# Kernel optimization log

Measured on AMD Instinct MI355X. Metric: run time of the kernel, lower is better.

The kernel has to match this reference:

```python
import jax, jax.numpy as jnp
import numpy as np

BETA = 0.25
TASK_LR = 1.0
EMBED_DIM = 256
DICT_SIZES = [64, 128, 256, 512]


def setup_inputs() -> dict:
    key = jax.random.key(0)
    ks = jax.random.split(key, 6)
    inp = {
        "x": jax.random.normal(ks[0], (16, 64, 64, EMBED_DIM), dtype=jnp.float32),
        "alpha_vq": jax.random.normal(ks[1], (4,), dtype=jnp.float32),
    }
    # RandomUniform default range (-0.05, 0.05)
    for i, n in enumerate(DICT_SIZES):
        inp[f"dict_{6 + i}"] = jax.random.uniform(
            ks[2 + i], (EMBED_DIM, n), dtype=jnp.float32, minval=-0.05, maxval=0.05
        )
    return inp


def _quantize(flat, dic):
    # flat: [N, D], dic: [D, K]
    sim = flat @ dic  # [N, K]
    dists = (
        jnp.sum(flat * flat, axis=1, keepdims=True)
        + jnp.sum(dic * dic, axis=0, keepdims=True)
        - 2.0 * sim
    )
    idx = jnp.argmin(dists, axis=1)  # [N]
    # equivalent to one_hot(idx) @ dic.T, but as a direct gather
    return jnp.take(dic.T, idx, axis=0)  # [N, D]


def reference(x, alpha_vq, dict_6, dict_7, dict_8, dict_9):
    dicts = [dict_6, dict_7, dict_8, dict_9]
    sg = jax.lax.stop_gradient
    alpha = jax.nn.softmax(alpha_vq)  # [4]
    flat = x.reshape(-1, EMBED_DIM)  # [N, D]

    qs, dict_losses, commit_losses = [], [], []
    for dic in dicts:
        q = _quantize(flat, dic)
        qs.append(q)
        dict_losses.append(jnp.mean(jnp.square(sg(flat) - q)))
        commit_losses.append(jnp.mean(jnp.square(flat - sg(q))))

    loss = jnp.sum(jnp.stack(dict_losses) * alpha) + BETA * jnp.sum(
        jnp.stack(commit_losses) * alpha
    )

    weighted_q = jnp.sum(jnp.stack(qs, axis=0) * alpha[:, None, None], axis=0)
    weighted_q = (TASK_LR * weighted_q).reshape(x.shape)
    # straight-through estimator
    weighted_q = x + sg(weighted_q - x)
    return weighted_q, loss
```

## Files before the change

### kernel.cpp

```cpp
#include <hip/hip_runtime.h>
#include <float.h>
#include <math.h>

#define D 256
#define NROWS 65536
#define RPB 64
#define EPS_CAND 0.02f
#define CAP 6
#define WSFRAG 1024
#define WSDT   246784
#define ASTRIDE 520


typedef __attribute__((ext_vector_type(8)))  short short8v;
typedef __attribute__((ext_vector_type(16))) float f32x16;
typedef __attribute__((ext_vector_type(4)))  float float4v;
typedef __attribute__((ext_vector_type(4)))  uint  uint4v;

__device__ __forceinline__ ushort f2bf(float v) {
    uint u = __float_as_uint(v);
    u += 0x7fffu + ((u >> 16) & 1u);
    return (ushort)(u >> 16);
}
__device__ __forceinline__ float bf2f(ushort u) { return __uint_as_float(((uint)u) << 16); }

__device__ __forceinline__ int fidx(int ct, int c, int s, int half, int j, int p) {
    return ((ct * 16 + s) * 2 + p) * 512 + (c + 32 * half) * 8 + j;
}
__device__ __forceinline__ float dget(const ushort* fr, int pc, int d) {
    int b = fidx(pc >> 5, pc & 31, d >> 4, (d >> 3) & 1, d & 7, 0);
    return bf2f(fr[b]) + bf2f(fr[b + 512]);
}
__device__ __forceinline__ void dic_sel(int pc, const float* dc0, const float* dc1,
                                        const float* dc2, const float* dc3,
                                        const float*& dic, int& K, int& kk) {
    if      (pc < 64)  { dic = dc0; K = 64;  kk = pc;       }
    else if (pc < 192) { dic = dc1; K = 128; kk = pc - 64;  }
    else if (pc < 448) { dic = dc2; K = 256; kk = pc - 192; }
    else               { dic = dc3; K = 512; kk = pc - 448; }
}

__global__ void vq_prep(const float* __restrict__ av,
                        const float* __restrict__ dc0, const float* __restrict__ dc1,
                        const float* __restrict__ dc2, const float* __restrict__ dc3,
                        float* __restrict__ ws, float* __restrict__ dT)
{
    int t = blockIdx.x * 256 + threadIdx.x;
    ushort* fr = (ushort*)(ws + WSFRAG);
    if (t == 0) {
        double x0 = av[0], x1 = av[1], x2 = av[2], x3 = av[3];
        double m = fmax(fmax(x0, x1), fmax(x2, x3));
        double e0 = exp(x0 - m), e1 = exp(x1 - m), e2 = exp(x2 - m), e3 = exp(x3 - m);
        double inv = 1.0 / (e0 + e1 + e2 + e3);
        ws[0] = (float)(e0 * inv); ws[1] = (float)(e1 * inv);
        ws[2] = (float)(e2 * inv); ws[3] = (float)(e3 * inv);
        double* lacc = (double*)(ws + 968);
        lacc[0] = 0.0; lacc[1] = 0.0; lacc[2] = 0.0; lacc[3] = 0.0;
        double* dal = (double*)(ws + 976);
        dal[0] = e0 * inv; dal[1] = e1 * inv; dal[2] = e2 * inv; dal[3] = e3 * inv;
    }
    if (t < 960) {
        const float* dic; int K, kk;
        dic_sel(t, dc0, dc1, dc2, dc3, dic, K, kk);
        float s = 0.0f;
        if (dT != nullptr) {
            float* dr = dT + (size_t)t * D;
            for (int d = 0; d < D; ++d) {
                float v = dic[d * K + kk];
                s = __fadd_rn(s, __fmul_rn(v, v));
                dr[d] = v;
            }
        } else {
            for (int d = 0; d < D; ++d) {
                float v = dic[d * K + kk];
                s = __fadd_rn(s, __fmul_rn(v, v));
            }
        }
        ws[4 + t] = s;
    }
    if (t < 7680) {
        int pc = t >> 3;
        const float* dic; int K, kk;
        dic_sel(pc, dc0, dc1, dc2, dc3, dic, K, kk);
        int ct = pc >> 5, c = pc & 31;
        int kb = (t & 7) * 32;
        for (int k = kb; k < kb + 32; ++k) {
            float v = dic[k * K + kk];
            ushort hu = f2bf(v);
            ushort lu = f2bf(v - bf2f(hu));
            fr[fidx(ct, c, k >> 4, (k >> 3) & 1, k & 7, 0)] = hu;
            fr[fidx(ct, c, k >> 4, (k >> 3) & 1, k & 7, 1)] = lu;
        }
    }
}

__device__ __forceinline__ void load_Bh(short8v (&B)[2], const ushort* bfr, int ct0, int s, int lane) {
#pragma unroll
    for (int cc = 0; cc < 2; ++cc)
        B[cc] = *(const short8v*)&bfr[(((ct0 + cc) * 16 + s) * 2) * 512 + lane * 8];
}
__device__ __forceinline__ void load_Ah(short8v (&A)[2], const ushort* af, int s, int lane) {
#pragma unroll
    for (int rt = 0; rt < 2; ++rt)
        A[rt] = *(const short8v*)&af[(rt * 16 + s) * ASTRIDE + lane * 8];
}

template<class F>
__device__ __forceinline__ void gemm_group(const ushort* af, const ushort* bfr,
                                           int ct0, int lane, float c2A, float c2B, F&& emit)
{
    f32x16 acc[2][2];
#pragma unroll
    for (int a = 0; a < 2; ++a)
#pragma unroll
        for (int b = 0; b < 2; ++b) acc[a][b] = (f32x16)(0.0f);

    short8v A[3][2], B[8][2];
#pragma unroll
    for (int s = 0; s < 7; ++s) load_Bh(B[s], bfr, ct0, s, lane);
    load_Ah(A[0], af, 0, lane);
    load_Ah(A[1], af, 1, lane);
#pragma unroll
    for (int s = 0; s < 16; ++s) {
        if (s + 7 < 16) load_Bh(B[(s + 7) & 7], bfr, ct0, s + 7, lane);
        if (s + 2 < 16) load_Ah(A[(s + 2) % 3], af, s + 2, lane);
        const int ai = s % 3, bi = s & 7;
#pragma unroll
        for (int rt = 0; rt < 2; ++rt)
#pragma unroll
            for (int cc = 0; cc < 2; ++cc)
                acc[rt][cc] = __builtin_amdgcn_mfma_f32_32x32x16_bf16(A[ai][rt], B[bi][cc], acc[rt][cc], 0, 0, 0);
    }
#pragma unroll
    for (int rt = 0; rt < 2; ++rt)
#pragma unroll
        for (int reg = 0; reg < 16; ++reg)
            emit(rt, reg, fmaf(-2.0f, acc[rt][0][reg], c2A), fmaf(-2.0f, acc[rt][1][reg], c2B));
}

__global__ void __launch_bounds__(256, 2) vq_main(
    const float* __restrict__ x,
    const float* __restrict__ dc0, const float* __restrict__ dc1,
    const float* __restrict__ dc2, const float* __restrict__ dc3,
    float* __restrict__ ws, const float* __restrict__ dT, float* __restrict__ out)
{
    __shared__ double lred[4][4];
    __shared__ __align__(16) ushort afrag[32 * ASTRIDE];
    __shared__ float slotmin[5][64];
    __shared__ float thrL[4][64];
    __shared__ float f2row[64];
    __shared__ int   cnt[4][64];
    __shared__ int   cand[4][64][CAP];
    __shared__ int   kfin[4][64];
    __shared__ int   rep_list[64];
    __shared__ int   rep_cnt;

    const int tid  = threadIdx.x;
    const int lane = tid & 63;
    const int wv   = __builtin_amdgcn_readfirstlane(tid >> 6);
    const int lcol = lane & 31, half = lane >> 5;
    const size_t rowbase = (size_t)blockIdx.x * RPB;

    if (tid == 0) rep_cnt = 0;
    for (int i = tid; i < 256; i += 256) { (&cnt[0][0])[i] = 0; }

    const float4v* x4 = (const float4v*)(x + rowbase * D);
    for (int it = 0; it < 8; ++it) {
        int f = it * 256 + tid;
        int row = f >> 5, sh = f & 31, s = sh >> 1, hf = sh & 1;
        float4v va = __builtin_nontemporal_load(&x4[row * 64 + s * 4 + hf * 2]);
        float4v vb = __builtin_nontemporal_load(&x4[row * 64 + s * 4 + hf * 2 + 1]);
        ushort h[8];
#pragma unroll
        for (int i = 0; i < 4; ++i) {
            h[i]     = f2bf(va[i]);
            h[4 + i] = f2bf(vb[i]);
        }
        int bu = ((row >> 5) * 16 + s) * ASTRIDE + ((row & 31) + 32 * hf) * 8;
        uint4v Hv = { (uint)h[0] | ((uint)h[1] << 16), (uint)h[2] | ((uint)h[3] << 16),
                      (uint)h[4] | ((uint)h[5] << 16), (uint)h[6] | ((uint)h[7] << 16) };
        *(uint4v*)&afrag[bu] = Hv;
    }
    __syncthreads();

    if (tid < 64) {
        const float* xr = x + (rowbase + tid) * D;
        double s = 0.0;
        for (int d0 = 0; d0 < D; d0 += 4) {
            float4v v = *(const float4v*)&xr[d0];
#pragma unroll
            for (int j = 0; j < 4; ++j) s = fma((double)v[j], (double)v[j], s);
        }
        f2row[tid] = (float)s;
    }

    const ushort* bfr = (const ushort*)(ws + WSFRAG);
    const float*  c2  = ws + 4;
    const int ngroups = (wv == 0) ? 3 : 4;

    {
        float rv1[2][16];
#pragma unroll
        for (int rt = 0; rt < 2; ++rt)
#pragma unroll
            for (int r = 0; r < 16; ++r) rv1[rt][r] = FLT_MAX;

        for (int g = 0; g < ngroups; ++g) {
            const int ct0 = (wv == 0) ? 2 * g : 6 + (wv - 1) * 8 + 2 * g;
            gemm_group(afrag, bfr, ct0, lane, c2[ct0 * 32 + lcol], c2[ct0 * 32 + 32 + lcol],
                [&](int rt, int reg, float sA, float sB) {
                    rv1[rt][reg] = fminf(rv1[rt][reg], fminf(sA, sB));
                });
            const bool doflush = (wv == 0) ? (g == 0 || g == 2) : (g == 3);
            if (doflush) {
                const int slot = (wv == 0) ? ((g == 0) ? 0 : 1) : wv + 1;
#pragma unroll
                for (int rt = 0; rt < 2; ++rt)
#pragma unroll
                    for (int r = 0; r < 16; ++r) {
                        float v = rv1[rt][r];
#pragma unroll
                        for (int off = 1; off <= 16; off <<= 1) v = fminf(v, __shfl_xor(v, off));
                        if (lcol == r)
                            slotmin[slot][rt * 32 + (r & 3) + 8 * (r >> 2) + 4 * half] = v;
                        rv1[rt][r] = FLT_MAX;
                    }
            }
        }
    }
    __syncthreads();

    {
        int i = tid >> 6, r = tid & 63;
        float m1 = (i < 3) ? slotmin[i][r] : fminf(slotmin[3][r], slotmin[4][r]);
        thrL[i][r] = m1 + EPS_CAND;
    }
    __syncthreads();

    for (int g = 0; g < ngroups; ++g) {
        const int ct0 = (wv == 0) ? 2 * g : 6 + (wv - 1) * 8 + 2 * g;
        const int dct = (wv == 0) ? ((g == 0) ? 0 : 1) : ((wv == 1) ? 2 : 3);
        gemm_group(afrag, bfr, ct0, lane, c2[ct0 * 32 + lcol], c2[ct0 * 32 + 32 + lcol],
            [&](int rt, int reg, float sA, float sB) {
                const int row = rt * 32 + (reg & 3) + 8 * (reg >> 2) + 4 * half;
                const float thr = thrL[dct][row];
                if (sA < thr) {
                    int pos = atomicAdd(&cnt[dct][row], 1);
                    if (pos < CAP) cand[dct][row][pos] = ct0 * 32 + lcol;
                }
                if (sB < thr) {
                    int pos = atomicAdd(&cnt[dct][row], 1);
                    if (pos < CAP) cand[dct][row][pos] = ct0 * 32 + 32 + lcol;
                }
            });
    }
    __syncthreads();

    {
        const int i = tid >> 6, r = tid & 63;
        const int n = cnt[i][r];
        if (n > CAP) {
            int p = atomicAdd(&rep_cnt, 1);
            rep_list[p] = (i << 6) | r;
        } else {
            const float f2 = f2row[r];
            const float* xrow = x + (rowbase + r) * D;
            float best = FLT_MAX; int bi = 0x7fffffff;
            for (int j = 0; j < n; ++j) {
                const int pc = cand[i][r][j];
                double smd = 0.0;
                if (dT != nullptr) {
                    const float* br = dT + (size_t)pc * D;
                    for (int d0 = 0; d0 < D; d0 += 4) {
                        float4v xa = *(const float4v*)&xrow[d0];
                        float4v bb = *(const float4v*)&br[d0];
#pragma unroll
                        for (int j2 = 0; j2 < 4; ++j2)
                            smd = fma((double)xa[j2], (double)bb[j2], smd);
                    }
                } else {
                    for (int d0 = 0; d0 < D; d0 += 8) {
                        float4v xa = *(const float4v*)&xrow[d0];
                        float4v xb = *(const float4v*)&xrow[d0 + 4];
                        int bb = fidx(pc >> 5, pc & 31, d0 >> 4, (d0 >> 3) & 1, 0, 0);
                        short8v bh = *(const short8v*)&bfr[bb];
                        short8v bl = *(const short8v*)&bfr[bb + 512];
#pragma unroll
                        for (int j2 = 0; j2 < 4; ++j2) {
                            double bv0 = (double)(bf2f((ushort)bh[j2]) + bf2f((ushort)bl[j2]));
                            double bv1 = (double)(bf2f((ushort)bh[4 + j2]) + bf2f((ushort)bl[4 + j2]));
                            smd = fma((double)xa[j2], bv0, smd);
                            smd = fma((double)xb[j2], bv1, smd);
                        }
                    }
                }
                float sim  = (float)smd;
                float dist = __fsub_rn(__fadd_rn(f2, c2[pc]), __fmul_rn(2.0f, sim));
                if (dist < best || (dist == best && pc < bi)) { best = dist; bi = pc; }
            }
            kfin[i][r] = bi;
        }
    }
    __syncthreads();

    for (int t = wv; t < rep_cnt; t += 4) {
        int e = rep_list[t];
        int i = e >> 6, r = e & 63;
        const float* dic; int K, base;
        if      (i == 0) { dic = dc0; K = 64;  base = 0;   }
        else if (i == 1) { dic = dc1; K = 128; base = 64;  }
        else if (i == 2) { dic = dc2; K = 256; base = 192; }
        else             { dic = dc3; K = 512; base = 448; }
        const float* xrow = x + (rowbase + r) * D;
        const float f2 = f2row[r];
        float bestv = FLT_MAX; int besti = 0x7fffffff;
        for (int c = lane; c < K; c += 64) {
            float  cn  = 0.0f;
            double smd = 0.0;
            for (int d = 0; d < D; ++d) {
                float bv = dic[d * K + c];
                cn  = __fadd_rn(cn, __fmul_rn(bv, bv));
                smd = fma((double)xrow[d], (double)bv, smd);
            }
            float sim  = (float)smd;
            float dist = __fsub_rn(__fadd_rn(f2, cn), __fmul_rn(2.0f, sim));
            if (dist < bestv) { bestv = dist; besti = c; }
        }
#pragma unroll
        for (int off = 32; off; off >>= 1) {
            float ov = __shfl_xor(bestv, off);
            int   oi = __shfl_xor(besti, off);
            if (ov < bestv || (ov == bestv && oi < besti)) { bestv = ov; besti = oi; }
        }
        if (lane == 0) kfin[i][r] = base + besti;
    }
    __syncthreads();

    const float a0 = ws[0], a1 = ws[1], a2 = ws[2], a3 = ws[3];
    double l0 = 0.0, l1 = 0.0, l2 = 0.0, l3 = 0.0;
#pragma unroll 4
    for (int r = 0; r < RPB; ++r) {
        const float xv = x[(rowbase + r) * D + tid];
        const int i0 = kfin[0][r], i1 = kfin[1][r], i2 = kfin[2][r], i3 = kfin[3][r];
        float q0, q1, q2, q3;
        if (dT != nullptr) {
            q0 = dT[(size_t)i0 * D + tid];
            q1 = dT[(size_t)i1 * D + tid];
            q2 = dT[(size_t)i2 * D + tid];
            q3 = dT[(size_t)i3 * D + tid];
        } else {
            q0 = dget(bfr, i0, tid);
            q1 = dget(bfr, i1, tid);
            q2 = dget(bfr, i2, tid);
            q3 = dget(bfr, i3, tid);
        }
        float wq = __fadd_rn(__fadd_rn(__fadd_rn(__fmul_rn(a0, q0), __fmul_rn(a1, q1)),
                                       __fmul_rn(a2, q2)), __fmul_rn(a3, q3));
        __builtin_nontemporal_store(__fadd_rn(xv, __fsub_rn(wq, xv)),
                                    &out[(rowbase + r) * D + tid]);
        const float e0 = xv - q0, e1 = xv - q1, e2 = xv - q2, e3 = xv - q3;
        l0 = fma((double)e0, (double)e0, l0);
        l1 = fma((double)e1, (double)e1, l1);
        l2 = fma((double)e2, (double)e2, l2);
        l3 = fma((double)e3, (double)e3, l3);
    }
#pragma unroll
    for (int off = 32; off; off >>= 1) {
        l0 += __shfl_down(l0, off); l1 += __shfl_down(l1, off);
        l2 += __shfl_down(l2, off); l3 += __shfl_down(l3, off);
    }
    if (lane == 0) { lred[wv][0] = l0; lred[wv][1] = l1; lred[wv][2] = l2; lred[wv][3] = l3; }
    __syncthreads();
    if (tid == 0) {
        double* lacc = (double*)(ws + 968);
#pragma unroll
        for (int i = 0; i < 4; ++i)
            atomicAdd(lacc + i, lred[0][i] + lred[1][i] + lred[2][i] + lred[3][i]);
    }
}

__global__ void vq_fin(const float* __restrict__ ws, float* __restrict__ out)
{
    if (threadIdx.x == 0) {
        const double* lacc = (const double*)(ws + 968);
        const double* dal  = (const double*)(ws + 976);
        double s = 0.0;
#pragma unroll
        for (int i = 0; i < 4; ++i) s += (lacc[i] * (1.0 / 16777216.0)) * dal[i];
        out[16777216] = (float)(s + 0.25 * s);
    }
}

extern "C" void kernel_launch(void* const* d_in, const int* in_sizes, int n_in,
                              void* d_out, int out_size, void* d_ws, size_t ws_size,
                              hipStream_t stream)
{
    const float* x   = (const float*)d_in[0];
    const float* av  = (const float*)d_in[1];
    const float* dc0 = (const float*)d_in[2];
    const float* dc1 = (const float*)d_in[3];
    const float* dc2 = (const float*)d_in[4];
    const float* dc3 = (const float*)d_in[5];
    float* out = (float*)d_out;
    float* ws  = (float*)d_ws;

    const bool haveDT = ws_size >= (size_t)(WSDT + 960 * 256) * sizeof(float);
    float* dT = haveDT ? (ws + WSDT) : nullptr;

    hipLaunchKernelGGL(vq_prep, dim3(30), dim3(256), 0, stream, av, dc0, dc1, dc2, dc3, ws, dT);
    hipLaunchKernelGGL(vq_main, dim3(NROWS / RPB), dim3(256), 0, stream,
                       x, dc0, dc1, dc2, dc3, ws, dT, out);
    hipLaunchKernelGGL(vq_fin, dim3(1), dim3(64), 0, stream, ws, out);
}
```

Measured before the change: 287.4 us.

## Split VQ kernel into score and epilogue kernels with single-tile GEMM passes

Splits the fused kernel into a scoring kernel that writes the chosen codeword indices to workspace and a separate epilogue kernel that gathers codewords, writes the output and accumulates the losses. The GEMM is restructured from 2-column-tile groups with deep register prefetch to one 32-column tile per step, with contiguous tile ranges per wave. Together with a smaller candidate cap and shared-memory aliasing, this cuts register and LDS use so that launch bounds can ask for 4 blocks per SM instead of 2. The cost is an extra kernel launch, a second read of x, a round trip of the indices through global memory, and less operand reuse per MFMA.

```diff
diff --git a/kernel.cpp b/kernel.cpp
--- a/kernel.cpp
+++ b/kernel.cpp
@@ -6,9 +6,10 @@
 #define NROWS 65536
 #define RPB 64
 #define EPS_CAND 0.02f
-#define CAP 6
+#define CAP 4
 #define WSFRAG 1024
-#define WSDT   246784
+#define WSKF   246784
+#define WSDT   377856
 #define ASTRIDE 520
 
 
@@ -94,66 +95,52 @@
     }
 }
 
-__device__ __forceinline__ void load_Bh(short8v (&B)[2], const ushort* bfr, int ct0, int s, int lane) {
-#pragma unroll
-    for (int cc = 0; cc < 2; ++cc)
-        B[cc] = *(const short8v*)&bfr[(((ct0 + cc) * 16 + s) * 2) * 512 + lane * 8];
-}
-__device__ __forceinline__ void load_Ah(short8v (&A)[2], const ushort* af, int s, int lane) {
-#pragma unroll
-    for (int rt = 0; rt < 2; ++rt)
-        A[rt] = *(const short8v*)&af[(rt * 16 + s) * ASTRIDE + lane * 8];
-}
-
-template<class F>
-__device__ __forceinline__ void gemm_group(const ushort* af, const ushort* bfr,
-                                           int ct0, int lane, float c2A, float c2B, F&& emit)
-{
-    f32x16 acc[2][2];
-#pragma unroll
-    for (int a = 0; a < 2; ++a)
-#pragma unroll
-        for (int b = 0; b < 2; ++b) acc[a][b] = (f32x16)(0.0f);
-
-    short8v A[3][2], B[8][2];
-#pragma unroll
-    for (int s = 0; s < 7; ++s) load_Bh(B[s], bfr, ct0, s, lane);
-    load_Ah(A[0], af, 0, lane);
-    load_Ah(A[1], af, 1, lane);
-#pragma unroll
-    for (int s = 0; s < 16; ++s) {
-        if (s + 7 < 16) load_Bh(B[(s + 7) & 7], bfr, ct0, s + 7, lane);
-        if (s + 2 < 16) load_Ah(A[(s + 2) % 3], af, s + 2, lane);
-        const int ai = s % 3, bi = s & 7;
-#pragma unroll
-        for (int rt = 0; rt < 2; ++rt)
-#pragma unroll
-            for (int cc = 0; cc < 2; ++cc)
-                acc[rt][cc] = __builtin_amdgcn_mfma_f32_32x32x16_bf16(A[ai][rt], B[bi][cc], acc[rt][cc], 0, 0, 0);
-    }
-#pragma unroll
-    for (int rt = 0; rt < 2; ++rt)
-#pragma unroll
-        for (int reg = 0; reg < 16; ++reg)
-            emit(rt, reg, fmaf(-2.0f, acc[rt][0][reg], c2A), fmaf(-2.0f, acc[rt][1][reg], c2B));
-}
-
-__global__ void __launch_bounds__(256, 2) vq_main(
+__device__ __forceinline__ short8v load_B1(const ushort* bfr, int t, int s, int lane) {
+    return *(const short8v*)&bfr[((t * 16 + s) * 2) * 512 + lane * 8];
+}
+__device__ __forceinline__ void load_A1(short8v (&A)[2], const ushort* af, int s, int lane) {
+    A[0] = *(const short8v*)&af[(0 * 16 + s) * ASTRIDE + lane * 8];
+    A[1] = *(const short8v*)&af[(1 * 16 + s) * ASTRIDE + lane * 8];
+}
+
+template<class FE>
+__device__ __forceinline__ void gemm_pass(const ushort* af, const ushort* bfr,
+                                          int ts, int te, int lane, FE&& emit_tile)
+{
+    short8v A[2][2], B[4];
+    load_A1(A[0], af, 0, lane);
+    B[0] = load_B1(bfr, ts, 0, lane);
+    B[1] = load_B1(bfr, ts, 1, lane);
+    B[2] = load_B1(bfr, ts, 2, lane);
+    for (int kt = ts; kt < te; ++kt) {
+        f32x16 acc0 = (f32x16)(0.0f), acc1 = (f32x16)(0.0f);
+#pragma unroll
+        for (int s = 0; s < 16; ++s) {
+            const int pt = kt + ((s + 3) >> 4);
+            if (pt < te) B[(s + 3) & 3] = load_B1(bfr, pt, (s + 3) & 15, lane);
+            load_A1(A[(s + 1) & 1], af, (s + 1) & 15, lane);
+            acc0 = __builtin_amdgcn_mfma_f32_32x32x16_bf16(A[s & 1][0], B[s & 3], acc0, 0, 0, 0);
+            acc1 = __builtin_amdgcn_mfma_f32_32x32x16_bf16(A[s & 1][1], B[s & 3], acc1, 0, 0, 0);
+        }
+        emit_tile(kt, acc0, acc1);
+    }
+}
+
+__global__ void __launch_bounds__(256, 4) vq_score(
     const float* __restrict__ x,
     const float* __restrict__ dc0, const float* __restrict__ dc1,
     const float* __restrict__ dc2, const float* __restrict__ dc3,
-    float* __restrict__ ws, const float* __restrict__ dT, float* __restrict__ out)
-{
-    __shared__ double lred[4][4];
+    float* __restrict__ ws, const float* __restrict__ dT, ushort* __restrict__ wkf)
+{
     __shared__ __align__(16) ushort afrag[32 * ASTRIDE];
-    __shared__ float slotmin[5][64];
+    __shared__ int   cand[4][64][CAP];
     __shared__ float thrL[4][64];
     __shared__ float f2row[64];
     __shared__ int   cnt[4][64];
-    __shared__ int   cand[4][64][CAP];
-    __shared__ int   kfin[4][64];
     __shared__ int   rep_list[64];
     __shared__ int   rep_cnt;
+
+    float* slotminp = (float*)&cand[0][0][0];
 
     const int tid  = threadIdx.x;
     const int lane = tid & 63;
@@ -162,7 +149,7 @@
     const size_t rowbase = (size_t)blockIdx.x * RPB;
 
     if (tid == 0) rep_cnt = 0;
-    for (int i = tid; i < 256; i += 256) { (&cnt[0][0])[i] = 0; }
+    for (int i = tid; i < 256; i += 256) (&cnt[0][0])[i] = 0;
 
     const float4v* x4 = (const float4v*)(x + rowbase * D);
     for (int it = 0; it < 8; ++it) {
@@ -172,10 +159,7 @@
         float4v vb = __builtin_nontemporal_load(&x4[row * 64 + s * 4 + hf * 2 + 1]);
         ushort h[8];
 #pragma unroll
-        for (int i = 0; i < 4; ++i) {
-            h[i]     = f2bf(va[i]);
-            h[4 + i] = f2bf(vb[i]);
-        }
+        for (int i = 0; i < 4; ++i) { h[i] = f2bf(va[i]); h[4 + i] = f2bf(vb[i]); }
         int bu = ((row >> 5) * 16 + s) * ASTRIDE + ((row & 31) + 32 * hf) * 8;
         uint4v Hv = { (uint)h[0] | ((uint)h[1] << 16), (uint)h[2] | ((uint)h[3] << 16),
                       (uint)h[4] | ((uint)h[5] << 16), (uint)h[6] | ((uint)h[7] << 16) };
@@ -195,67 +179,75 @@
     }
 
     const ushort* bfr = (const ushort*)(ws + WSFRAG);
-    const float*  c2  = ws + 4;
-    const int ngroups = (wv == 0) ? 3 : 4;
+    const float*  c2g = ws + 4;
+    const int ts = (wv == 0) ? 0 : (wv == 1) ? 7 : (wv == 2) ? 14 : 22;
+    const int te = (wv == 0) ? 7 : (wv == 1) ? 14 : (wv == 2) ? 22 : 30;
 
     {
-        float rv1[2][16];
-#pragma unroll
-        for (int rt = 0; rt < 2; ++rt)
-#pragma unroll
-            for (int r = 0; r < 16; ++r) rv1[rt][r] = FLT_MAX;
-
-        for (int g = 0; g < ngroups; ++g) {
-            const int ct0 = (wv == 0) ? 2 * g : 6 + (wv - 1) * 8 + 2 * g;
-            gemm_group(afrag, bfr, ct0, lane, c2[ct0 * 32 + lcol], c2[ct0 * 32 + 32 + lcol],
-                [&](int rt, int reg, float sA, float sB) {
-                    rv1[rt][reg] = fminf(rv1[rt][reg], fminf(sA, sB));
-                });
-            const bool doflush = (wv == 0) ? (g == 0 || g == 2) : (g == 3);
-            if (doflush) {
-                const int slot = (wv == 0) ? ((g == 0) ? 0 : 1) : wv + 1;
-#pragma unroll
-                for (int rt = 0; rt < 2; ++rt)
-#pragma unroll
-                    for (int r = 0; r < 16; ++r) {
-                        float v = rv1[rt][r];
-#pragma unroll
-                        for (int off = 1; off <= 16; off <<= 1) v = fminf(v, __shfl_xor(v, off));
-                        if (lcol == r)
-                            slotmin[slot][rt * 32 + (r & 3) + 8 * (r >> 2) + 4 * half] = v;
-                        rv1[rt][r] = FLT_MAX;
-                    }
-            }
-        }
+        float rv0[16], rv1a[16];
+#pragma unroll
+        for (int r = 0; r < 16; ++r) { rv0[r] = FLT_MAX; rv1a[r] = FLT_MAX; }
+        gemm_pass(afrag, bfr, ts, te, lane,
+            [&](int kt, const f32x16& a0, const f32x16& a1) {
+                const float c2t = c2g[kt * 32 + lcol];
+#pragma unroll
+                for (int reg = 0; reg < 16; ++reg) {
+                    rv0[reg]  = fminf(rv0[reg],  fmaf(-2.0f, a0[reg], c2t));
+                    rv1a[reg] = fminf(rv1a[reg], fmaf(-2.0f, a1[reg], c2t));
+                }
+                int slot = -1;
+                if      (kt == 1)  slot = 0;
+                else if (kt == 5)  slot = 1;
+                else if (kt == 6)  slot = 2;
+                else if (kt == 13) slot = 3;
+                else if (kt == 21) slot = 4;
+                else if (kt == 29) slot = 5;
+                if (slot >= 0) {
+#pragma unroll
+                    for (int rt = 0; rt < 2; ++rt)
+#pragma unroll
+                        for (int reg = 0; reg < 16; ++reg) {
+                            float v = rt ? rv1a[reg] : rv0[reg];
+#pragma unroll
+                            for (int off = 1; off <= 16; off <<= 1) v = fminf(v, __shfl_xor(v, off));
+                            if (lcol == reg)
+                                slotminp[slot * 64 + rt * 32 + (reg & 3) + 8 * (reg >> 2) + 4 * half] = v;
+                            if (rt) rv1a[reg] = FLT_MAX; else rv0[reg] = FLT_MAX;
+                        }
+                }
+            });
     }
     __syncthreads();
 
     {
         int i = tid >> 6, r = tid & 63;
-        float m1 = (i < 3) ? slotmin[i][r] : fminf(slotmin[3][r], slotmin[4][r]);
+        float m1 = (i == 0) ? slotminp[r]
+                 : (i == 1) ? slotminp[64 + r]
+                 : (i == 2) ? fminf(slotminp[128 + r], slotminp[192 + r])
+                            : fminf(slotminp[256 + r], slotminp[320 + r]);
         thrL[i][r] = m1 + EPS_CAND;
     }
     __syncthreads();
 
-    for (int g = 0; g < ngroups; ++g) {
-        const int ct0 = (wv == 0) ? 2 * g : 6 + (wv - 1) * 8 + 2 * g;
-        const int dct = (wv == 0) ? ((g == 0) ? 0 : 1) : ((wv == 1) ? 2 : 3);
-        gemm_group(afrag, bfr, ct0, lane, c2[ct0 * 32 + lcol], c2[ct0 * 32 + 32 + lcol],
-            [&](int rt, int reg, float sA, float sB) {
-                const int row = rt * 32 + (reg & 3) + 8 * (reg >> 2) + 4 * half;
-                const float thr = thrL[dct][row];
-                if (sA < thr) {
-                    int pos = atomicAdd(&cnt[dct][row], 1);
-                    if (pos < CAP) cand[dct][row][pos] = ct0 * 32 + lcol;
+    gemm_pass(afrag, bfr, ts, te, lane,
+        [&](int kt, const f32x16& a0, const f32x16& a1) {
+            const float c2t = c2g[kt * 32 + lcol];
+            const int dct = (kt < 2) ? 0 : (kt < 6) ? 1 : (kt < 14) ? 2 : 3;
+#pragma unroll
+            for (int rt = 0; rt < 2; ++rt)
+#pragma unroll
+                for (int reg = 0; reg < 16; ++reg) {
+                    float sc = fmaf(-2.0f, rt ? a1[reg] : a0[reg], c2t);
+                    const int row = rt * 32 + (reg & 3) + 8 * (reg >> 2) + 4 * half;
+                    if (sc < thrL[dct][row]) {
+                        int pos = atomicAdd(&cnt[dct][row], 1);
+                        if (pos < CAP) cand[dct][row][pos] = kt * 32 + lcol;
+                    }
                 }
-                if (sB < thr) {
-                    int pos = atomicAdd(&cnt[dct][row], 1);
-                    if (pos < CAP) cand[dct][row][pos] = ct0 * 32 + 32 + lcol;
-                }
-            });
-    }
-    __syncthreads();
-
+        });
+    __syncthreads();
+
+    ushort* kf = wkf + (size_t)blockIdx.x * 256;
     {
         const int i = tid >> 6, r = tid & 63;
         const int n = cnt[i][r];
@@ -295,10 +287,10 @@
                     }
                 }
                 float sim  = (float)smd;
-                float dist = __fsub_rn(__fadd_rn(f2, c2[pc]), __fmul_rn(2.0f, sim));
+                float dist = __fsub_rn(__fadd_rn(f2, c2g[pc]), __fmul_rn(2.0f, sim));
                 if (dist < best || (dist == best && pc < bi)) { best = dist; bi = pc; }
             }
-            kfin[i][r] = bi;
+            kf[i * 64 + r] = (ushort)bi;
         }
     }
     __syncthreads();
@@ -332,16 +324,32 @@
             int   oi = __shfl_xor(besti, off);
             if (ov < bestv || (ov == bestv && oi < besti)) { bestv = ov; besti = oi; }
         }
-        if (lane == 0) kfin[i][r] = base + besti;
-    }
+        if (lane == 0) kf[i * 64 + r] = (ushort)(base + besti);
+    }
+}
+
+__global__ void vq_epi(const float* __restrict__ x, float* __restrict__ ws,
+                       const float* __restrict__ dT, const ushort* __restrict__ wkf,
+                       float* __restrict__ out)
+{
+    __shared__ double lred[4][4];
+    __shared__ int kf[256];
+
+    const int tid  = threadIdx.x;
+    const int lane = tid & 63;
+    const int wv   = __builtin_amdgcn_readfirstlane(tid >> 6);
+    const size_t rowbase = (size_t)blockIdx.x * RPB;
+    const ushort* bfr = (const ushort*)(ws + WSFRAG);
+
+    kf[tid] = wkf[(size_t)blockIdx.x * 256 + tid];
     __syncthreads();
 
     const float a0 = ws[0], a1 = ws[1], a2 = ws[2], a3 = ws[3];
     double l0 = 0.0, l1 = 0.0, l2 = 0.0, l3 = 0.0;
 #pragma unroll 4
     for (int r = 0; r < RPB; ++r) {
-        const float xv = x[(rowbase + r) * D + tid];
-        const int i0 = kfin[0][r], i1 = kfin[1][r], i2 = kfin[2][r], i3 = kfin[3][r];
+        const float xv = __builtin_nontemporal_load(&x[(rowbase + r) * D + tid]);
+        const int i0 = kf[r], i1 = kf[64 + r], i2 = kf[128 + r], i3 = kf[192 + r];
         float q0, q1, q2, q3;
         if (dT != nullptr) {
             q0 = dT[(size_t)i0 * D + tid];
@@ -404,11 +412,13 @@
     float* out = (float*)d_out;
     float* ws  = (float*)d_ws;
 
+    ushort* wkf = (ushort*)(ws + WSKF);
     const bool haveDT = ws_size >= (size_t)(WSDT + 960 * 256) * sizeof(float);
     float* dT = haveDT ? (ws + WSDT) : nullptr;
 
     hipLaunchKernelGGL(vq_prep, dim3(30), dim3(256), 0, stream, av, dc0, dc1, dc2, dc3, ws, dT);
-    hipLaunchKernelGGL(vq_main, dim3(NROWS / RPB), dim3(256), 0, stream,
-                       x, dc0, dc1, dc2, dc3, ws, dT, out);
+    hipLaunchKernelGGL(vq_score, dim3(NROWS / RPB), dim3(256), 0, stream,
+                       x, dc0, dc1, dc2, dc3, ws, dT, wkf);
+    hipLaunchKernelGGL(vq_epi, dim3(NROWS / RPB), dim3(256), 0, stream, x, ws, dT, wkf, out);
     hipLaunchKernelGGL(vq_fin, dim3(1), dim3(64), 0, stream, ws, out);
 }
```

Result: slower. 497.0 us (+72.9%).
